# Optimization experiments

Hardware: AMD Instinct MI355X
Metric: run time of the kernel (lower is better)

Reference implementation:

```python
import jax, jax.numpy as jnp
import numpy as np

NUM_CLASSES = 8192
FEAT_DIM = 256
BATCH = 1024
TEMPERATURE = 0.1
BASE_TEMPERATURE = 0.1
PROTO_M = 0.5
EPS = 1e-12  # F.normalize eps


def setup_inputs() -> dict:
    key = jax.random.key(0)
    k1, k2, k3 = jax.random.split(key, 3)
    features = jax.random.normal(k1, (BATCH, FEAT_DIM), dtype=jnp.float32)
    proto = jax.random.normal(k2, (NUM_CLASSES, FEAT_DIM), dtype=jnp.float32)
    # prototypes buffer is unit-normalized after init_class_prototypes
    proto = proto / jnp.maximum(jnp.linalg.norm(proto, axis=1, keepdims=True), EPS)
    labels = jax.random.randint(k3, (BATCH,), 0, NUM_CLASSES, dtype=jnp.int64)
    return {"features": features, "prototypes": proto, "labels": labels}


def _forward(features, prototypes, labels):
    # Sequential per-sample EMA prototype update (order matters for repeated labels)
    def step(proto, fc):
        f, c = fc
        row = proto[c] * PROTO_M + f * (1.0 - PROTO_M)
        row = row / jnp.maximum(jnp.linalg.norm(row), EPS)
        return proto.at[c].set(row), None

    proto, _ = jax.lax.scan(step, prototypes, (features, labels))

    # Pairwise prototype similarity, masked (off-diagonal) mean of exp, then log
    logits = jnp.matmul(proto, proto.T) / TEMPERATURE          # [C, C]
    C = proto.shape[0]
    mask = 1.0 - jnp.eye(C, dtype=logits.dtype)                # zero diagonal
    neg_sum = jnp.sum(mask * jnp.exp(logits), axis=1)          # [C]
    mean_prob_neg = jnp.log(neg_sum / jnp.sum(mask, axis=1))
    # torch drops NaN rows before mean; nanmean reproduces that
    loss = (TEMPERATURE / BASE_TEMPERATURE) * jnp.nanmean(mean_prob_neg)
    return loss


def reference(features, prototypes, labels):
    return _forward(features, prototypes, labels)
```

## Files before the change

kernel.cpp:

```cpp
#include <hip/hip_runtime.h>
#include <hip/hip_bf16.h>
#include <math.h>

#define NUM_CLASSES 8192
#define FEAT_DIM    256
#define BATCH       1024

typedef long fp8x8;
typedef __attribute__((ext_vector_type(4))) float f32x4;

#define GLD16(gp, lp) __builtin_amdgcn_global_load_lds(                       \
    (const __attribute__((address_space(1))) void*)(gp),                      \
    (__attribute__((address_space(3))) void*)(lp), 16, 0, 0)

__global__ __launch_bounds__(256) void ema_convert_kernel(
    const float* __restrict__ feats, const float* __restrict__ proto,
    const int* __restrict__ labels, unsigned char* __restrict__ P8,
    float* __restrict__ rowsum) {
  __shared__ int lab_s[BATCH];
  const int tid = threadIdx.x;

  ((int4*)lab_s)[tid] = ((const int4*)labels)[tid];
  if (blockIdx.x < 32) rowsum[blockIdx.x * 256 + tid] = 0.0f;
  __syncthreads();

  const int c    = (blockIdx.x << 2) + (tid >> 6);
  const int lane = tid & 63;

  float4 p = ((const float4*)(proto + (size_t)c * FEAT_DIM))[lane];

  const int4 L0 = ((const int4*)lab_s)[lane * 4 + 0];
  const int4 L1 = ((const int4*)lab_s)[lane * 4 + 1];
  const int4 L2 = ((const int4*)lab_s)[lane * 4 + 2];
  const int4 L3 = ((const int4*)lab_s)[lane * 4 + 3];
  unsigned m = 0;
  m |= (L0.x == c) << 0;  m |= (L0.y == c) << 1;
  m |= (L0.z == c) << 2;  m |= (L0.w == c) << 3;
  m |= (L1.x == c) << 4;  m |= (L1.y == c) << 5;
  m |= (L1.z == c) << 6;  m |= (L1.w == c) << 7;
  m |= (L2.x == c) << 8;  m |= (L2.y == c) << 9;
  m |= (L2.z == c) << 10; m |= (L2.w == c) << 11;
  m |= (L3.x == c) << 12; m |= (L3.y == c) << 13;
  m |= (L3.z == c) << 14; m |= (L3.w == c) << 15;

  unsigned long long wm = __ballot(m != 0);
  while (wm) {
    const int src = __ffsll((long long)wm) - 1;
    unsigned mm = __shfl(m, src);
    while (mm) {
      const int j = __ffs(mm) - 1;
      mm &= mm - 1;
      const int t = src * 16 + j;
      float4 f = ((const float4*)(feats + (size_t)t * FEAT_DIM))[lane];
      float4 r;
      r.x = 0.5f * p.x + 0.5f * f.x;
      r.y = 0.5f * p.y + 0.5f * f.y;
      r.z = 0.5f * p.z + 0.5f * f.z;
      r.w = 0.5f * p.w + 0.5f * f.w;
      float ss = r.x * r.x + r.y * r.y + r.z * r.z + r.w * r.w;
#pragma unroll
      for (int off = 32; off; off >>= 1) ss += __shfl_xor(ss, off);
      float inv = 1.0f / fmaxf(sqrtf(ss), 1e-12f);
      p.x = r.x * inv; p.y = r.y * inv; p.z = r.z * inv; p.w = r.w * inv;
    }
    wm &= wm - 1;
  }

  int v = __builtin_amdgcn_cvt_pk_fp8_f32(p.x, p.y, 0, false);
  v = __builtin_amdgcn_cvt_pk_fp8_f32(p.z, p.w, v, true);
  ((int*)(P8 + (size_t)c * FEAT_DIM))[lane] = v;
}

#define BM 128
#define NB (NUM_CLASSES / BM)
#define NTRI (NB * (NB + 1) / 2)
#define NBLK (NTRI / 2)
#define LROW 128

__global__ __launch_bounds__(256, 4) void gemm_rowsum_kernel(
    const unsigned char* __restrict__ P8, float* __restrict__ rowsum) {
  __shared__ __align__(16) char As[BM * LROW];
  __shared__ __align__(16) char Bs[BM * LROW];
  __shared__ float Lrow[2][2][BM];
  __shared__ float Lcol[2][2][BM];

  const int hw  = blockIdx.x;
  const int bid = (hw & 7) * (NBLK / 8) + (hw >> 3);

  int rem = bid * 2, bi0 = 0;
  while (rem >= (NB - bi0)) { rem -= (NB - bi0); ++bi0; }
  const int bj0 = bi0 + rem;
  const int bi1 = (bj0 + 1 < NB) ? bi0 : bi0 + 1;
  const int bj1 = (bj0 + 1 < NB) ? bj0 + 1 : bi0 + 1;

  const int tid  = threadIdx.x;
  const int wid  = tid >> 6;
  const int lane = tid & 63;
  const int wm   = wid >> 1;
  const int wn   = wid & 1;

  f32x4 acc[4][4] = {};

  const int rloc = lane >> 3;
  const int csrc = (lane & 7) ^ rloc;
  const unsigned char* PA = P8 + (size_t)(bi0 * BM) * FEAT_DIM;
  const unsigned char* PB = P8 + (size_t)(bj0 * BM) * FEAT_DIM;

#define STAGE(kt)                                                             \
  {                                                                           \
    _Pragma("unroll")                                                         \
    for (int q = 0; q < 4; ++q) {                                             \
      const int L = wid * 4 + q;                                   \
      const int r = L * 8 + rloc;                        \
      const size_t go = (size_t)r * FEAT_DIM + (kt) * 128 + csrc * 16;        \
      GLD16(PA + go, As + L * 1024);                                          \
      GLD16(PB + go, Bs + L * 1024);                                          \
    }                                                                         \
  }

  const int g  = lane >> 4;
  const int rl = lane & 15;

#define COMPUTE()                                                             \
  {                                                                           \
    _Pragma("unroll")                                                         \
    for (int kk = 0; kk < 4; ++kk) {                                          \
      const int cl = 2 * kk + (g >> 1);                \
      const int ib = (g & 1) * 8;                             \
      fp8x8 a[4], b[4];                                                       \
      _Pragma("unroll")                                                       \
      for (int mi = 0; mi < 4; ++mi) {                                        \
        const int row = wm * 64 + mi * 16 + rl;                               \
        a[mi] = *(const fp8x8*)(As + row * LROW + ((cl ^ (row & 7)) << 4) + ib);\
      }                                                                       \
      _Pragma("unroll")                                                       \
      for (int ni = 0; ni < 4; ++ni) {                                        \
        const int row = wn * 64 + ni * 16 + rl;                               \
        b[ni] = *(const fp8x8*)(Bs + row * LROW + ((cl ^ (row & 7)) << 4) + ib);\
      }                                                                       \
      _Pragma("unroll")                                                       \
      for (int mi = 0; mi < 4; ++mi)                                          \
        _Pragma("unroll")                                                     \
        for (int ni = 0; ni < 4; ++ni)                                        \
          acc[mi][ni] = __builtin_amdgcn_mfma_f32_16x16x32_fp8_fp8(           \
              a[mi], b[ni], acc[mi][ni], 0, 0, 0);                            \
    }                                                                         \
  }

#define EPI_CALC(T, BI, BJ)                                                   \
  {                                                                           \
    const bool diag = ((BI) == (BJ));                                         \
    float col[4] = {0.0f, 0.0f, 0.0f, 0.0f};                                  \
    _Pragma("unroll")                                                         \
    for (int mi = 0; mi < 4; ++mi) {                                          \
      _Pragma("unroll")                                                       \
      for (int v = 0; v < 4; ++v) {                                           \
        const int lrow = wm * 64 + mi * 16 + g * 4 + v;                       \
        const int grow = (BI) * BM + lrow;                                    \
        float rs = 0.0f;                                                      \
        _Pragma("unroll")                                                     \
        for (int ni = 0; ni < 4; ++ni) {                                      \
          const int gcol = (BJ) * BM + wn * 64 + ni * 16 + rl;                \
          float e = __expf(10.0f * acc[mi][ni][v]);                           \
          if (diag && grow == gcol) e = 0.0f;                                 \
          rs += e;                                                            \
          col[ni] += e;                                                       \
        }                                                                     \
        rs += __shfl_xor(rs, 1);                                              \
        rs += __shfl_xor(rs, 2);                                              \
        rs += __shfl_xor(rs, 4);                                              \
        rs += __shfl_xor(rs, 8);                                              \
        if (rl == 0) Lrow[T][wn][lrow] = rs;                                  \
      }                                                                       \
    }                                                                         \
    _Pragma("unroll")                                                         \
    for (int ni = 0; ni < 4; ++ni) {                                          \
      float cs = col[ni];                                                     \
      cs += __shfl_xor(cs, 16);                                               \
      cs += __shfl_xor(cs, 32);                                               \
      if (g == 0) Lcol[T][wm][wn * 64 + ni * 16 + rl] = cs;                   \
    }                                                                         \
  }

#define ZEROACC()                                                             \
  {                                                                           \
    _Pragma("unroll")                                                         \
    for (int mi = 0; mi < 4; ++mi)                                            \
      _Pragma("unroll")                                                       \
      for (int ni = 0; ni < 4; ++ni)                                          \
        acc[mi][ni] = (f32x4){0.0f, 0.0f, 0.0f, 0.0f};                        \
  }

  STAGE(0);
  __syncthreads();

  COMPUTE();
  __syncthreads();
  STAGE(1);
  __syncthreads();
  COMPUTE();
  __syncthreads();
  PA = P8 + (size_t)(bi1 * BM) * FEAT_DIM;
  PB = P8 + (size_t)(bj1 * BM) * FEAT_DIM;
  STAGE(0);
  EPI_CALC(0, bi0, bj0);
  ZEROACC();
  __syncthreads();
  COMPUTE();
  __syncthreads();
  STAGE(1);
  __syncthreads();
  COMPUTE();
  EPI_CALC(1, bi1, bj1);
  __syncthreads();

  {
    const int T = tid >> 7;
    const int r = tid & 127;
    const int biT = T ? bi1 : bi0;
    const int bjT = T ? bj1 : bj0;
    atomicAdd(&rowsum[biT * BM + r], Lrow[T][0][r] + Lrow[T][1][r]);
    if (biT != bjT)
      atomicAdd(&rowsum[bjT * BM + r], Lcol[T][0][r] + Lcol[T][1][r]);
  }
}

__global__ __launch_bounds__(256) void finalize_kernel(
    const float* __restrict__ rowsum, float* __restrict__ out) {
  const int tid = threadIdx.x;
  float s = 0.0f;
  for (int i = tid; i < NUM_CLASSES; i += 256) {
    s += logf(rowsum[i] * (1.0f / (float)(NUM_CLASSES - 1)));
  }
#pragma unroll
  for (int off = 32; off; off >>= 1) s += __shfl_xor(s, off);
  __shared__ float red[4];
  if ((tid & 63) == 0) red[tid >> 6] = s;
  __syncthreads();
  if (tid == 0)
    out[0] = (red[0] + red[1] + red[2] + red[3]) * (1.0f / (float)NUM_CLASSES);
}

extern "C" void kernel_launch(void* const* d_in, const int* in_sizes, int n_in,
                              void* d_out, int out_size, void* d_ws, size_t ws_size,
                              hipStream_t stream) {
  const float* feats  = (const float*)d_in[0];
  const float* proto  = (const float*)d_in[1];
  const int*   labels = (const int*)d_in[2];
  float*       out    = (float*)d_out;

  char* ws = (char*)d_ws;
  unsigned char* P8 = (unsigned char*)ws;
  float* rowsum = (float*)(ws + (size_t)NUM_CLASSES * FEAT_DIM);

  ema_convert_kernel<<<NUM_CLASSES / 4, 256, 0, stream>>>(feats, proto, labels,
                                                          P8, rowsum);
  gemm_rowsum_kernel<<<NBLK, 256, 0, stream>>>(P8, rowsum);
  finalize_kernel<<<1, 256, 0, stream>>>(rowsum, out);
}
```

Measured before the change: 61.05 us.

## Keep a 128-row A panel resident and stream chains of B tiles

The GEMM kernel now loads a 128-row by 256-byte A panel into LDS once per block. It then walks a chain of up to eight 64-column B tiles over the upper triangle, double-buffering the B loads across K halves. Row sums accumulate in LDS across the whole chain and are flushed with one atomic per row, which cuts A reloads and global atomic traffic. The costs are more LDS per block, a lower occupancy hint, uneven chain lengths across blocks, and a grid of 544 blocks instead of 1040.

```diff
diff --git a/kernel.cpp b/kernel.cpp
--- a/kernel.cpp
+++ b/kernel.cpp
@@ -71,98 +71,114 @@
   ((int*)(P8 + (size_t)c * FEAT_DIM))[lane] = v;
 }
 
-#define BM 128
-#define NB (NUM_CLASSES / BM)
-#define NTRI (NB * (NB + 1) / 2)
-#define NBLK (NTRI / 2)
-#define LROW 128
-
-__global__ __launch_bounds__(256, 4) void gemm_rowsum_kernel(
+#define NCHAIN 544
+
+__global__ __launch_bounds__(256, 3) void gemm_rowsum_kernel(
     const unsigned char* __restrict__ P8, float* __restrict__ rowsum) {
-  __shared__ __align__(16) char As[BM * LROW];
-  __shared__ __align__(16) char Bs[BM * LROW];
-  __shared__ float Lrow[2][2][BM];
-  __shared__ float Lcol[2][2][BM];
+  __shared__ __align__(16) char As[128 * 256];
+  __shared__ __align__(16) char Bs[2][64 * 128];
+  __shared__ float Lrow[2][128];
+  __shared__ float Lcol[8][64];
 
   const int hw  = blockIdx.x;
-  const int bid = (hw & 7) * (NBLK / 8) + (hw >> 3);
-
-  int rem = bid * 2, bi0 = 0;
-  while (rem >= (NB - bi0)) { rem -= (NB - bi0); ++bi0; }
-  const int bj0 = bi0 + rem;
-  const int bi1 = (bj0 + 1 < NB) ? bi0 : bi0 + 1;
-  const int bj1 = (bj0 + 1 < NB) ? bj0 + 1 : bi0 + 1;
+  const int bid = (hw & 7) * (NCHAIN / 8) + (hw >> 3);
+
+  int I = 0, rem = bid;
+  while (rem >= ((64 - I + 3) >> 2)) { rem -= (64 - I + 3) >> 2; ++I; }
+  const int Jstart = 2 * I + rem * 8;
+  const int Lc = min(8, 128 - 2 * I - rem * 8);
 
   const int tid  = threadIdx.x;
   const int wid  = tid >> 6;
   const int lane = tid & 63;
   const int wm   = wid >> 1;
   const int wn   = wid & 1;
-
-  f32x4 acc[4][4] = {};
-
-  const int rloc = lane >> 3;
-  const int csrc = (lane & 7) ^ rloc;
-  const unsigned char* PA = P8 + (size_t)(bi0 * BM) * FEAT_DIM;
-  const unsigned char* PB = P8 + (size_t)(bj0 * BM) * FEAT_DIM;
-
-#define STAGE(kt)                                                             \
+  const int g    = lane >> 4;
+  const int rl   = lane & 15;
+
+  ((float*)Lrow)[tid] = 0.0f;
+  ((float*)Lcol)[tid] = 0.0f;
+  ((float*)Lcol)[tid + 256] = 0.0f;
+
+  {
+    const unsigned char* PA = P8 + (size_t)(I * 128) * FEAT_DIM;
+    const int rloc = lane >> 4;
+    const int cph  = lane & 15;
+#pragma unroll
+    for (int q = 0; q < 8; ++q) {
+      const int Ld = wid * 8 + q;
+      const int r  = Ld * 4 + rloc;
+      const int cs = cph ^ (r & 15);
+      GLD16(PA + (size_t)r * FEAT_DIM + cs * 16, As + Ld * 1024);
+    }
+  }
+
+  const int brloc = lane >> 3;
+  const int bcph  = lane & 7;
+#define SB(T, KT, BUF)                                                        \
   {                                                                           \
-    _Pragma("unroll")                                                         \
-    for (int q = 0; q < 4; ++q) {                                             \
-      const int L = wid * 4 + q;                                   \
-      const int r = L * 8 + rloc;                        \
-      const size_t go = (size_t)r * FEAT_DIM + (kt) * 128 + csrc * 16;        \
-      GLD16(PA + go, As + L * 1024);                                          \
-      GLD16(PB + go, Bs + L * 1024);                                          \
-    }                                                                         \
-  }
-
-  const int g  = lane >> 4;
-  const int rl = lane & 15;
-
-#define COMPUTE()                                                             \
+    const unsigned char* PB = P8 + (size_t)((Jstart + (T)) * 64) * FEAT_DIM;  \
+    _Pragma("unroll")                                                         \
+    for (int q = 0; q < 2; ++q) {                                             \
+      const int Ld = wid * 2 + q;                                   \
+      const int r  = Ld * 8 + brloc;                               \
+      const int cs = bcph ^ (r & 7);                                          \
+      GLD16(PB + (size_t)r * FEAT_DIM + (KT) * 128 + cs * 16,                 \
+            Bs[BUF] + Ld * 1024);                                             \
+    }                                                                         \
+  }
+
+  SB(0, 0, 0);
+  __syncthreads();
+
+  f32x4 acc[4][2] = {};
+
+#define COMPUTE(KT, BUF)                                                      \
   {                                                                           \
     _Pragma("unroll")                                                         \
     for (int kk = 0; kk < 4; ++kk) {                                          \
-      const int cl = 2 * kk + (g >> 1);                \
-      const int ib = (g & 1) * 8;                             \
-      fp8x8 a[4], b[4];                                                       \
+      const int ca = ((KT) * 4 + kk) * 2 + (g >> 1);       \
+      const int cb = kk * 2 + (g >> 1);                    \
+      const int ib = (g & 1) * 8;                                             \
+      fp8x8 a[4], b[2];                                                       \
       _Pragma("unroll")                                                       \
       for (int mi = 0; mi < 4; ++mi) {                                        \
         const int row = wm * 64 + mi * 16 + rl;                               \
-        a[mi] = *(const fp8x8*)(As + row * LROW + ((cl ^ (row & 7)) << 4) + ib);\
+        a[mi] = *(const fp8x8*)(As + row * 256 +                              \
+                                ((ca ^ (row & 15)) << 4) + ib);               \
       }                                                                       \
       _Pragma("unroll")                                                       \
-      for (int ni = 0; ni < 4; ++ni) {                                        \
-        const int row = wn * 64 + ni * 16 + rl;                               \
-        b[ni] = *(const fp8x8*)(Bs + row * LROW + ((cl ^ (row & 7)) << 4) + ib);\
+      for (int ni = 0; ni < 2; ++ni) {                                        \
+        const int row = wn * 32 + ni * 16 + rl;                               \
+        b[ni] = *(const fp8x8*)(Bs[BUF] + row * 128 +                         \
+                                ((cb ^ (row & 7)) << 4) + ib);                \
       }                                                                       \
       _Pragma("unroll")                                                       \
       for (int mi = 0; mi < 4; ++mi)                                          \
         _Pragma("unroll")                                                     \
-        for (int ni = 0; ni < 4; ++ni)                                        \
+        for (int ni = 0; ni < 2; ++ni)                                        \
           acc[mi][ni] = __builtin_amdgcn_mfma_f32_16x16x32_fp8_fp8(           \
               a[mi], b[ni], acc[mi][ni], 0, 0, 0);                            \
     }                                                                         \
   }
 
-#define EPI_CALC(T, BI, BJ)                                                   \
+#define EPI(T)                                                                \
   {                                                                           \
-    const bool diag = ((BI) == (BJ));                                         \
-    float col[4] = {0.0f, 0.0f, 0.0f, 0.0f};                                  \
+    const int Jt = Jstart + (T);                                              \
+    const bool edge = ((Jt >> 1) == I);                                       \
+    float col[2] = {0.0f, 0.0f};                                              \
     _Pragma("unroll")                                                         \
     for (int mi = 0; mi < 4; ++mi) {                                          \
       _Pragma("unroll")                                                       \
       for (int v = 0; v < 4; ++v) {                                           \
         const int lrow = wm * 64 + mi * 16 + g * 4 + v;                       \
-        const int grow = (BI) * BM + lrow;                                    \
+        const int grow = I * 128 + lrow;                                      \
         float rs = 0.0f;                                                      \
         _Pragma("unroll")                                                     \
-        for (int ni = 0; ni < 4; ++ni) {                                      \
-          const int gcol = (BJ) * BM + wn * 64 + ni * 16 + rl;                \
+        for (int ni = 0; ni < 2; ++ni) {                                      \
+          const int gcol = Jt * 64 + wn * 32 + ni * 16 + rl;                  \
           float e = __expf(10.0f * acc[mi][ni][v]);                           \
-          if (diag && grow == gcol) e = 0.0f;                                 \
+          if (edge && grow == gcol) e = 0.0f;                                 \
           rs += e;                                                            \
           col[ni] += e;                                                       \
         }                                                                     \
@@ -170,58 +186,41 @@
         rs += __shfl_xor(rs, 2);                                              \
         rs += __shfl_xor(rs, 4);                                              \
         rs += __shfl_xor(rs, 8);                                              \
-        if (rl == 0) Lrow[T][wn][lrow] = rs;                                  \
+        if (rl == 0) Lrow[wn][lrow] += rs;         \
       }                                                                       \
     }                                                                         \
     _Pragma("unroll")                                                         \
-    for (int ni = 0; ni < 4; ++ni) {                                          \
+    for (int ni = 0; ni < 2; ++ni) {                                          \
       float cs = col[ni];                                                     \
       cs += __shfl_xor(cs, 16);                                               \
       cs += __shfl_xor(cs, 32);                                               \
-      if (g == 0) Lcol[T][wm][wn * 64 + ni * 16 + rl] = cs;                   \
-    }                                                                         \
-  }
-
-#define ZEROACC()                                                             \
-  {                                                                           \
-    _Pragma("unroll")                                                         \
-    for (int mi = 0; mi < 4; ++mi)                                            \
-      _Pragma("unroll")                                                       \
-      for (int ni = 0; ni < 4; ++ni)                                          \
-        acc[mi][ni] = (f32x4){0.0f, 0.0f, 0.0f, 0.0f};                        \
-  }
-
-  STAGE(0);
-  __syncthreads();
-
-  COMPUTE();
-  __syncthreads();
-  STAGE(1);
-  __syncthreads();
-  COMPUTE();
-  __syncthreads();
-  PA = P8 + (size_t)(bi1 * BM) * FEAT_DIM;
-  PB = P8 + (size_t)(bj1 * BM) * FEAT_DIM;
-  STAGE(0);
-  EPI_CALC(0, bi0, bj0);
-  ZEROACC();
-  __syncthreads();
-  COMPUTE();
-  __syncthreads();
-  STAGE(1);
-  __syncthreads();
-  COMPUTE();
-  EPI_CALC(1, bi1, bj1);
-  __syncthreads();
-
-  {
-    const int T = tid >> 7;
-    const int r = tid & 127;
-    const int biT = T ? bi1 : bi0;
-    const int bjT = T ? bj1 : bj0;
-    atomicAdd(&rowsum[biT * BM + r], Lrow[T][0][r] + Lrow[T][1][r]);
-    if (biT != bjT)
-      atomicAdd(&rowsum[bjT * BM + r], Lcol[T][0][r] + Lcol[T][1][r]);
+      if (g == 0)                                                             \
+        atomicAdd(&Lcol[T][wn * 32 + ni * 16 + rl], cs);        \
+    }                                                                         \
+  }
+
+  for (int t = 0; t < Lc; ++t) {
+    SB(t, 1, 1);
+    COMPUTE(0, 0);
+    __syncthreads();
+    if (t + 1 < Lc) SB(t + 1, 0, 0);
+    COMPUTE(1, 1);
+    EPI(t);
+#pragma unroll
+    for (int mi = 0; mi < 4; ++mi)
+#pragma unroll
+      for (int ni = 0; ni < 2; ++ni)
+        acc[mi][ni] = (f32x4){0.0f, 0.0f, 0.0f, 0.0f};
+    __syncthreads();
+  }
+
+  if (tid < 128)
+    atomicAdd(&rowsum[I * 128 + tid], Lrow[0][tid] + Lrow[1][tid]);
+  for (int idx = tid; idx < Lc * 64; idx += 256) {
+    const int t = idx >> 6, c = idx & 63;
+    const int Jt = Jstart + t;
+    if ((Jt >> 1) != I)
+      atomicAdd(&rowsum[Jt * 64 + c], Lcol[t][c]);
   }
 }
 
@@ -255,6 +254,6 @@
 
   ema_convert_kernel<<<NUM_CLASSES / 4, 256, 0, stream>>>(feats, proto, labels,
                                                           P8, rowsum);
-  gemm_rowsum_kernel<<<NBLK, 256, 0, stream>>>(P8, rowsum);
+  gemm_rowsum_kernel<<<NCHAIN, 256, 0, stream>>>(P8, rowsum);
   finalize_kernel<<<1, 256, 0, stream>>>(rowsum, out);
 }
```

Measured after the change: 71.15 us. 1.17x slower.
